# Kernel optimization log

Hardware: AMD Instinct MI355X
Metric: run time of the kernel (lower is better)

The kernel has to match this reference:

```python
import jax, jax.numpy as jnp
import numpy as np

N_BLADES = 8  # Cl(3,0): 1, e1, e2, e3 and their products (bitmask blade indexing)


def _blade_sign(a: int, b: int) -> int:
    # Sign from reordering basis vectors when multiplying blades a*b (Euclidean metric).
    a >>= 1
    s = 0
    while a:
        s += bin(a & b).count('1')
        a >>= 1
    return -1 if (s & 1) else 1


def make_cayley() -> np.ndarray:
    C = np.zeros((N_BLADES, N_BLADES, N_BLADES), dtype=np.float32)
    for a in range(N_BLADES):
        for b in range(N_BLADES):
            C[a, b, a ^ b] = float(_blade_sign(a, b))
    return C


def setup_inputs() -> dict:
    key = jax.random.key(0)
    k1, k2 = jax.random.split(key)
    B, Cin, Cout = 8192, 256, 256
    scale = 1.0 / np.sqrt(Cin * N_BLADES)
    x = jax.random.normal(k1, (B, Cin, N_BLADES), dtype=jnp.float32)
    weight = jax.random.normal(k2, (Cout, Cin, N_BLADES), dtype=jnp.float32) * scale
    bias = jnp.zeros((Cout, N_BLADES), dtype=jnp.float32)
    cayley = jnp.asarray(make_cayley())
    return {"x": x, "weight": weight, "bias": bias, "cayley": cayley}


def reference(x, weight, bias, cayley):
    # A[b,o,j,k] = sum_i W[o,i,j] * X[b,i,k]  (weight blade j times input blade k)
    A = jnp.einsum('oij,bik->bojk', weight, x)
    # Contract blade pair (j,k) into output blade l via sparse Cayley table.
    out = jnp.einsum('jkl,bojk->bol', cayley, A)
    return out + bias[None, :, :]
```

## Files before the change

### kernel.cpp

```cpp
#include <hip/hip_runtime.h>
#include <stdint.h>
#include <stddef.h>


typedef __bf16 bf16x4 __attribute__((ext_vector_type(4)));
typedef __bf16 bf16x8 __attribute__((ext_vector_type(8)));
typedef float  f32x4  __attribute__((ext_vector_type(4)));
typedef float  f32x16 __attribute__((ext_vector_type(16)));

#define BM 256
#define BN 256
#define NSLICES 64
#define SLOT 8192

__device__ __forceinline__ void async_copy16(void* lds_dst, const void* g_src) {
    __builtin_amdgcn_global_load_lds(
        (__attribute__((address_space(1))) void*)g_src,
        (__attribute__((address_space(3))) void*)lds_dst,
        16, 0, 0);
}

__global__ __launch_bounds__(256) void prep_kernel(
    const float* __restrict__ x, __bf16* __restrict__ Xb2,
    const float* __restrict__ W, const float* __restrict__ cayley,
    __bf16* __restrict__ Wt2, int M, int N, int K, int Cin, int castBlocks)
{
    if ((int)blockIdx.x < castBlocks) {
        __shared__ __bf16 T[16 * 520];
        const int tk = blockIdx.x & 15;
        const int tm = blockIdx.x >> 4;
        const int row0 = tm * 64, k0 = tk * 128;
        #pragma unroll
        for (int it = 0; it < 8; ++it) {
            int idx = threadIdx.x + it * 256;
            int r = idx >> 5, kq = idx & 31;
            f32x4 v = *(const f32x4*)(x + (size_t)(row0 + r) * K + k0 + kq * 4);
            bf16x4 b;
            b[0] = (__bf16)v[0]; b[1] = (__bf16)v[1];
            b[2] = (__bf16)v[2]; b[3] = (__bf16)v[3];
            *(bf16x4*)&T[(kq >> 1) * 520 + r * 8 + (kq & 1) * 4] = b;
        }
        __syncthreads();
        const size_t obase = (size_t)(row0 >> 8) * K * 256
                           + (size_t)(k0 >> 3) * 2048
                           + (size_t)(row0 & 255) * 8;
        #pragma unroll
        for (int it = 0; it < 4; ++it) {
            int u = threadIdx.x + it * 256;
            int koL = u >> 6, rowi = u & 63;
            bf16x8 val = *(const bf16x8*)&T[koL * 520 + rowi * 8];
            *(bf16x8*)(Xb2 + obase + (size_t)koL * 2048 + rowi * 8) = val;
        }
        return;
    }
    __shared__ float Cay[512];
    for (int t = threadIdx.x; t < 512; t += 256) Cay[t] = cayley[t];
    __syncthreads();

    int flat = ((int)blockIdx.x - castBlocks) * 256 + threadIdx.x;
    if (flat >= Cin * N) return;
    int n = flat % N;
    int i = flat / N;
    int o = n >> 3, l = n & 7;

    const float* wrow = W + ((size_t)o * Cin + i) * 8;
    float w8[8];
    #pragma unroll
    for (int j = 0; j < 8; ++j) w8[j] = wrow[j];

    bf16x8 outv;
    #pragma unroll
    for (int k = 0; k < 8; ++k) {
        float s = 0.f;
        #pragma unroll
        for (int j = 0; j < 8; ++j) s += Cay[j * 64 + k * 8 + l] * w8[j];
        outv[k] = (__bf16)s;
    }
    *(bf16x8*)(Wt2 + (size_t)(n >> 8) * K * 256 + (size_t)i * 2048
                   + (n & 255) * 8) = outv;
}

__global__ __launch_bounds__(512, 2) void gemm_bt_kernel(
    const __bf16* __restrict__ A2,
    const __bf16* __restrict__ B2,
    const float*  __restrict__ bias,
    float* __restrict__ C,
    int M, int N, int K)
{
    __shared__ __align__(16) __bf16 As[4][SLOT];
    __shared__ __align__(16) __bf16 Bs[4][SLOT];

    const int tid  = threadIdx.x;
    const int wave = tid >> 6;
    const int lane = tid & 63;
    const int l31  = lane & 31;
    const int lhi  = lane >> 5;

    const int bid = blockIdx.x;
    const int xcd = bid & 7;
    const int idx = bid >> 3;
    const int mBase = (xcd * 4 + (idx & 3)) * BM;
    const int nBase = (idx >> 2) * BN;

    const int c0 = 2 * wave, c1 = 2 * wave + 1;
    const __bf16* gA0 = A2 + (size_t)mBase * K + c0 * 512 + lane * 8;
    const __bf16* gA1 = A2 + (size_t)mBase * K + c1 * 512 + lane * 8;
    const __bf16* gB0 = B2 + (size_t)nBase * K + c0 * 512 + lane * 8;
    const __bf16* gB1 = B2 + (size_t)nBase * K + c1 * 512 + lane * 8;
    const int dstA0 = c0 * 512, dstA1 = c1 * 512;

#define STAGE_A(slot, q) do {                                              \
        async_copy16(&As[slot][dstA0], gA0 + (size_t)(q) * 8192);          \
        async_copy16(&As[slot][dstA1], gA1 + (size_t)(q) * 8192);          \
    } while (0)
#define STAGE_B(slot, q) do {                                              \
        async_copy16(&Bs[slot][dstA0], gB0 + (size_t)(q) * 8192);          \
        async_copy16(&Bs[slot][dstA1], gB1 + (size_t)(q) * 8192);          \
    } while (0)

    const int wm = wave >> 2;
    const int wn = wave & 3;
    const __bf16* paBase = &As[0][lhi * 2048 + (wm * 128 + l31) * 8];
    const __bf16* pbBase = &Bs[0][lhi * 2048 + (wn * 64  + l31) * 8];

    f32x16 acc[4][2] = {};
    bf16x8 a0A[4], b0A[2], a0B[4], b0B[2], af1[4], bf1[2];

    STAGE_A(0, 0); STAGE_B(0, 0);
    STAGE_A(1, 1); STAGE_B(1, 1);
    STAGE_A(2, 2); STAGE_B(2, 2);
    asm volatile("s_waitcnt vmcnt(8)" ::: "memory");
    __builtin_amdgcn_s_barrier();

    #pragma unroll
    for (int j = 0; j < 4; ++j)
        a0A[j] = *(const bf16x8*)(paBase + j * 256);
    #pragma unroll
    for (int q = 0; q < 2; ++q)
        b0A[q] = *(const bf16x8*)(pbBase + q * 256);

#define SLICE_BODY(s_, c_, n_, A0F, B0F, A0N, B0N, DOA, DOB, DOPF, VM0)        \
    do {                                                                       \
        _Pragma("unroll")                                                      \
        for (int j = 0; j < 4; ++j)                                            \
            af1[j] = *(const bf16x8*)(paBase + (c_) * SLOT + 4096 + j * 256);  \
        _Pragma("unroll")                                                      \
        for (int q = 0; q < 2; ++q)                                            \
            bf1[q] = *(const bf16x8*)(pbBase + (c_) * SLOT + 4096 + q * 256);  \
        if (DOA) STAGE_A(((s_) + 3) & 3, (s_) + 3);                            \
        __builtin_amdgcn_s_setprio(1);                                         \
        _Pragma("unroll")                                                      \
        for (int j = 0; j < 4; ++j)                                            \
            _Pragma("unroll")                                                  \
            for (int q = 0; q < 2; ++q)                                        \
                acc[j][q] = __builtin_amdgcn_mfma_f32_32x32x16_bf16(           \
                    A0F[j], B0F[q], acc[j][q], 0, 0, 0);                       \
        __builtin_amdgcn_s_setprio(0);                                         \
        if (VM0) asm volatile("s_waitcnt vmcnt(0)" ::: "memory");              \
        else     asm volatile("s_waitcnt vmcnt(6)" ::: "memory");              \
        __builtin_amdgcn_s_barrier();                                          \
        if (DOPF) {                                                            \
            _Pragma("unroll")                                                  \
            for (int j = 0; j < 4; ++j)                                        \
                A0N[j] = *(const bf16x8*)(paBase + (n_) * SLOT + j * 256);     \
            _Pragma("unroll")                                                  \
            for (int q = 0; q < 2; ++q)                                        \
                B0N[q] = *(const bf16x8*)(pbBase + (n_) * SLOT + q * 256);     \
        }                                                                      \
        if (DOB) STAGE_B(((s_) + 3) & 3, (s_) + 3);                            \
        __builtin_amdgcn_s_setprio(1);                                         \
        _Pragma("unroll")                                                      \
        for (int j = 0; j < 4; ++j)                                            \
            _Pragma("unroll")                                                  \
            for (int q = 0; q < 2; ++q)                                        \
                acc[j][q] = __builtin_amdgcn_mfma_f32_32x32x16_bf16(           \
                    af1[j], bf1[q], acc[j][q], 0, 0, 0);                       \
        __builtin_amdgcn_s_setprio(0);                                         \
        __builtin_amdgcn_s_barrier();                                          \
    } while (0)

    #pragma unroll 1
    for (int s4 = 0; s4 < 15; ++s4) {
        const int s = s4 * 4;
        SLICE_BODY(s + 0, 0, 1, a0A, b0A, a0B, b0B, true, true, true, false);
        SLICE_BODY(s + 1, 1, 2, a0B, b0B, a0A, b0A, true, true, true, false);
        SLICE_BODY(s + 2, 2, 3, a0A, b0A, a0B, b0B, true, true, true, false);
        SLICE_BODY(s + 3, 3, 0, a0B, b0B, a0A, b0A, true, true, true, false);
    }
    SLICE_BODY(60, 0, 1, a0A, b0A, a0B, b0B, true,  true,  true,  false);
    SLICE_BODY(61, 1, 2, a0B, b0B, a0A, b0A, false, false, true,  true);
    SLICE_BODY(62, 2, 3, a0A, b0A, a0B, b0B, false, false, true,  true);
    SLICE_BODY(63, 3, 0, a0B, b0B, a0A, b0A, false, false, false, true);
    asm volatile("s_waitcnt vmcnt(0)" ::: "memory");

#undef SLICE_BODY
#undef STAGE_A
#undef STAGE_B

    float bv[2];
    #pragma unroll
    for (int q = 0; q < 2; ++q)
        bv[q] = bias[nBase + wn * 64 + q * 32 + l31];

    #pragma unroll
    for (int mt = 0; mt < 4; ++mt) {
        #pragma unroll
        for (int q = 0; q < 2; ++q) {
            const int col = nBase + wn * 64 + q * 32 + l31;
            #pragma unroll
            for (int r = 0; r < 16; ++r) {
                const int row = mBase + wm * 128 + mt * 32
                              + (r & 3) + 8 * (r >> 2) + 4 * lhi;
                C[(size_t)row * N + col] = acc[mt][q][r] + bv[q];
            }
        }
    }
}

extern "C" void kernel_launch(void* const* d_in, const int* in_sizes, int n_in,
                              void* d_out, int out_size, void* d_ws, size_t ws_size,
                              hipStream_t stream) {
    const float* x      = (const float*)d_in[0];
    const float* weight = (const float*)d_in[1];
    const float* bias   = (const float*)d_in[2];
    const float* cayley = (const float*)d_in[3];
    float* out = (float*)d_out;

    const int Cout = in_sizes[2] / 8;
    const int Cin  = in_sizes[1] / (Cout * 8);
    const int Bm   = in_sizes[0] / (Cin * 8);
    const int M = Bm;
    const int N = Cout * 8;
    const int K = Cin * 8;

    __bf16* Xb2 = (__bf16*)d_ws;
    __bf16* Wt2 = (__bf16*)((char*)d_ws + (size_t)M * K * 2);

    int castBlocks = (M / 64) * (K / 128);
    int foldBlocks = (Cin * N + 255) / 256;
    prep_kernel<<<castBlocks + foldBlocks, 256, 0, stream>>>(
        x, Xb2, weight, cayley, Wt2, M, N, K, Cin, castBlocks);

    int grid = (M / BM) * (N / BN);
    gemm_bt_kernel<<<grid, 512, 0, stream>>>(Xb2, Wt2, bias, out, M, N, K);
}
```

Baseline: 181.7 us.

## Fuse fp32-to-bf16 activation cast into GEMM A-tile loading

Removes the separate cast/relayout pass over x and instead has the GEMM load fp32 x directly into registers, convert to bf16 and write into the LDS A tiles, with the software pipeline reworked around register-staged loads. The fold kernel is restructured to stage weights through shared memory per block. This drops a full write and re-read of the bf16 activation copy but adds conversion work, register pressure and twice the A-side global traffic per GEMM block, since fp32 is reread by each of the 8 N-tiles.

```diff
diff --git a/kernel.cpp b/kernel.cpp
--- a/kernel.cpp
+++ b/kernel.cpp
@@ -3,14 +3,12 @@
 #include <stddef.h>
 
 
-typedef __bf16 bf16x4 __attribute__((ext_vector_type(4)));
 typedef __bf16 bf16x8 __attribute__((ext_vector_type(8)));
 typedef float  f32x4  __attribute__((ext_vector_type(4)));
 typedef float  f32x16 __attribute__((ext_vector_type(16)));
 
 #define BM 256
 #define BN 256
-#define NSLICES 64
 #define SLOT 8192
 
 __device__ __forceinline__ void async_copy16(void* lds_dst, const void* g_src) {
@@ -20,53 +18,39 @@
         16, 0, 0);
 }
 
-__global__ __launch_bounds__(256) void prep_kernel(
-    const float* __restrict__ x, __bf16* __restrict__ Xb2,
+__device__ __forceinline__ bf16x8 cvt2(f32x4 a, f32x4 b) {
+    bf16x8 r;
+    r[0] = (__bf16)a[0]; r[1] = (__bf16)a[1];
+    r[2] = (__bf16)a[2]; r[3] = (__bf16)a[3];
+    r[4] = (__bf16)b[0]; r[5] = (__bf16)b[1];
+    r[6] = (__bf16)b[2]; r[7] = (__bf16)b[3];
+    return r;
+}
+
+__global__ __launch_bounds__(256) void fold_kernel(
     const float* __restrict__ W, const float* __restrict__ cayley,
-    __bf16* __restrict__ Wt2, int M, int N, int K, int Cin, int castBlocks)
+    __bf16* __restrict__ Wt2, int Cin, int N, int K)
 {
-    if ((int)blockIdx.x < castBlocks) {
-        __shared__ __bf16 T[16 * 520];
-        const int tk = blockIdx.x & 15;
-        const int tm = blockIdx.x >> 4;
-        const int row0 = tm * 64, k0 = tk * 128;
-        #pragma unroll
-        for (int it = 0; it < 8; ++it) {
-            int idx = threadIdx.x + it * 256;
-            int r = idx >> 5, kq = idx & 31;
-            f32x4 v = *(const f32x4*)(x + (size_t)(row0 + r) * K + k0 + kq * 4);
-            bf16x4 b;
-            b[0] = (__bf16)v[0]; b[1] = (__bf16)v[1];
-            b[2] = (__bf16)v[2]; b[3] = (__bf16)v[3];
-            *(bf16x4*)&T[(kq >> 1) * 520 + r * 8 + (kq & 1) * 4] = b;
-        }
-        __syncthreads();
-        const size_t obase = (size_t)(row0 >> 8) * K * 256
-                           + (size_t)(k0 >> 3) * 2048
-                           + (size_t)(row0 & 255) * 8;
-        #pragma unroll
-        for (int it = 0; it < 4; ++it) {
-            int u = threadIdx.x + it * 256;
-            int koL = u >> 6, rowi = u & 63;
-            bf16x8 val = *(const bf16x8*)&T[koL * 520 + rowi * 8];
-            *(bf16x8*)(Xb2 + obase + (size_t)koL * 2048 + rowi * 8) = val;
-        }
-        return;
-    }
     __shared__ float Cay[512];
+    __shared__ float Wl[32][8];
+    const int b  = blockIdx.x;
+    const int i  = b >> 3;
+    const int n0 = (b & 7) * 256;
+    const int o0 = n0 >> 3;
+
     for (int t = threadIdx.x; t < 512; t += 256) Cay[t] = cayley[t];
+    if (threadIdx.x < 64) {
+        int o2 = threadIdx.x >> 1, half = threadIdx.x & 1;
+        *(f32x4*)&Wl[o2][half * 4] =
+            *(const f32x4*)(W + ((size_t)(o0 + o2) * Cin + i) * 8 + half * 4);
+    }
     __syncthreads();
 
-    int flat = ((int)blockIdx.x - castBlocks) * 256 + threadIdx.x;
-    if (flat >= Cin * N) return;
-    int n = flat % N;
-    int i = flat / N;
-    int o = n >> 3, l = n & 7;
-
-    const float* wrow = W + ((size_t)o * Cin + i) * 8;
+    const int t  = threadIdx.x;
+    const int o2 = t >> 3, l = t & 7;
     float w8[8];
     #pragma unroll
-    for (int j = 0; j < 8; ++j) w8[j] = wrow[j];
+    for (int j = 0; j < 8; ++j) w8[j] = Wl[o2][j];
 
     bf16x8 outv;
     #pragma unroll
@@ -76,12 +60,13 @@
         for (int j = 0; j < 8; ++j) s += Cay[j * 64 + k * 8 + l] * w8[j];
         outv[k] = (__bf16)s;
     }
-    *(bf16x8*)(Wt2 + (size_t)(n >> 8) * K * 256 + (size_t)i * 2048
-                   + (n & 255) * 8) = outv;
+    const int n = n0 + t;
+    *(bf16x8*)(Wt2 + (size_t)(n >> 8) * (size_t)K * 256
+                   + (size_t)i * 2048 + (size_t)(n & 255) * 8) = outv;
 }
 
 __global__ __launch_bounds__(512, 2) void gemm_bt_kernel(
-    const __bf16* __restrict__ A2,
+    const float*  __restrict__ X,
     const __bf16* __restrict__ B2,
     const float*  __restrict__ bias,
     float* __restrict__ C,
@@ -102,20 +87,30 @@
     const int mBase = (xcd * 4 + (idx & 3)) * BM;
     const int nBase = (idx >> 2) * BN;
 
+    const int arow = tid >> 1;
+    const int akh  = tid & 1;
+    const float* gX = X + (size_t)(mBase + arow) * K + akh * 16;
+    const int wd0 = (2 * akh) * 2048 + arow * 8;
+    const int wd1 = wd0 + 2048;
+
     const int c0 = 2 * wave, c1 = 2 * wave + 1;
-    const __bf16* gA0 = A2 + (size_t)mBase * K + c0 * 512 + lane * 8;
-    const __bf16* gA1 = A2 + (size_t)mBase * K + c1 * 512 + lane * 8;
     const __bf16* gB0 = B2 + (size_t)nBase * K + c0 * 512 + lane * 8;
     const __bf16* gB1 = B2 + (size_t)nBase * K + c1 * 512 + lane * 8;
-    const int dstA0 = c0 * 512, dstA1 = c1 * 512;
-
-#define STAGE_A(slot, q) do {                                              \
-        async_copy16(&As[slot][dstA0], gA0 + (size_t)(q) * 8192);          \
-        async_copy16(&As[slot][dstA1], gA1 + (size_t)(q) * 8192);          \
+    const int dstB0 = c0 * 512, dstB1 = c1 * 512;
+
+#define ISSUE_A(SET, q) do {                                   \
+        SET[0] = *(const f32x4*)(gX + (size_t)(q) * 32);       \
+        SET[1] = *(const f32x4*)(gX + (size_t)(q) * 32 + 4);   \
+        SET[2] = *(const f32x4*)(gX + (size_t)(q) * 32 + 8);   \
+        SET[3] = *(const f32x4*)(gX + (size_t)(q) * 32 + 12);  \
+    } while (0)
+#define CVT_WRITE(SET, slot) do {                              \
+        *(bf16x8*)&As[slot][wd0] = cvt2(SET[0], SET[1]);       \
+        *(bf16x8*)&As[slot][wd1] = cvt2(SET[2], SET[3]);       \
     } while (0)
 #define STAGE_B(slot, q) do {                                              \
-        async_copy16(&Bs[slot][dstA0], gB0 + (size_t)(q) * 8192);          \
-        async_copy16(&Bs[slot][dstA1], gB1 + (size_t)(q) * 8192);          \
+        async_copy16(&Bs[slot][dstB0], gB0 + (size_t)(q) * 8192);          \
+        async_copy16(&Bs[slot][dstB1], gB1 + (size_t)(q) * 8192);          \
     } while (0)
 
     const int wm = wave >> 2;
@@ -125,11 +120,18 @@
 
     f32x16 acc[4][2] = {};
     bf16x8 a0A[4], b0A[2], a0B[4], b0B[2], af1[4], bf1[2];
-
-    STAGE_A(0, 0); STAGE_B(0, 0);
-    STAGE_A(1, 1); STAGE_B(1, 1);
-    STAGE_A(2, 2); STAGE_B(2, 2);
+    f32x4 aE[4], aO[4];
+
+    ISSUE_A(aE, 0); ISSUE_A(aO, 1);
+    STAGE_B(0, 0);  STAGE_B(1, 1);
     asm volatile("s_waitcnt vmcnt(8)" ::: "memory");
+    CVT_WRITE(aE, 0);
+    asm volatile("s_waitcnt vmcnt(4)" ::: "memory");
+    CVT_WRITE(aO, 1);
+    ISSUE_A(aE, 2);
+    STAGE_B(2, 2);
+    asm volatile("s_waitcnt vmcnt(6)" ::: "memory");
+    asm volatile("s_waitcnt lgkmcnt(0)" ::: "memory");
     __builtin_amdgcn_s_barrier();
 
     #pragma unroll
@@ -139,7 +141,8 @@
     for (int q = 0; q < 2; ++q)
         b0A[q] = *(const bf16x8*)(pbBase + q * 256);
 
-#define SLICE_BODY(s_, c_, n_, A0F, B0F, A0N, B0N, DOA, DOB, DOPF, VM0)        \
+#define SLICE_BODY(s_, c_, n_, A0F, B0F, A0N, B0N, AIS, ACV,                   \
+                   DOA, DOCVT, DOPF, DOB, VMODE)                               \
     do {                                                                       \
         _Pragma("unroll")                                                      \
         for (int j = 0; j < 4; ++j)                                            \
@@ -147,7 +150,7 @@
         _Pragma("unroll")                                                      \
         for (int q = 0; q < 2; ++q)                                            \
             bf1[q] = *(const bf16x8*)(pbBase + (c_) * SLOT + 4096 + q * 256);  \
-        if (DOA) STAGE_A(((s_) + 3) & 3, (s_) + 3);                            \
+        if (DOA) ISSUE_A(AIS, (s_) + 3);                                       \
         __builtin_amdgcn_s_setprio(1);                                         \
         _Pragma("unroll")                                                      \
         for (int j = 0; j < 4; ++j)                                            \
@@ -156,9 +159,12 @@
                 acc[j][q] = __builtin_amdgcn_mfma_f32_32x32x16_bf16(           \
                     A0F[j], B0F[q], acc[j][q], 0, 0, 0);                       \
         __builtin_amdgcn_s_setprio(0);                                         \
-        if (VM0) asm volatile("s_waitcnt vmcnt(0)" ::: "memory");              \
-        else     asm volatile("s_waitcnt vmcnt(6)" ::: "memory");              \
         __builtin_amdgcn_s_barrier();                                          \
+        if ((VMODE) == 0) asm volatile("s_waitcnt vmcnt(6)" ::: "memory");     \
+        else if ((VMODE) == 1) asm volatile("s_waitcnt vmcnt(2)" ::: "memory");\
+        else if ((VMODE) == 2) asm volatile("s_waitcnt vmcnt(0)" ::: "memory");\
+        if (DOB) STAGE_B(((s_) + 3) & 3, (s_) + 3);                            \
+        if (DOCVT) CVT_WRITE(ACV, ((s_) + 2) & 3);                             \
         if (DOPF) {                                                            \
             _Pragma("unroll")                                                  \
             for (int j = 0; j < 4; ++j)                                        \
@@ -167,7 +173,6 @@
             for (int q = 0; q < 2; ++q)                                        \
                 B0N[q] = *(const bf16x8*)(pbBase + (n_) * SLOT + q * 256);     \
         }                                                                      \
-        if (DOB) STAGE_B(((s_) + 3) & 3, (s_) + 3);                            \
         __builtin_amdgcn_s_setprio(1);                                         \
         _Pragma("unroll")                                                      \
         for (int j = 0; j < 4; ++j)                                            \
@@ -176,26 +181,27 @@
                 acc[j][q] = __builtin_amdgcn_mfma_f32_32x32x16_bf16(           \
                     af1[j], bf1[q], acc[j][q], 0, 0, 0);                       \
         __builtin_amdgcn_s_setprio(0);                                         \
+        asm volatile("s_waitcnt lgkmcnt(0)" ::: "memory");                     \
         __builtin_amdgcn_s_barrier();                                          \
     } while (0)
 
     #pragma unroll 1
     for (int s4 = 0; s4 < 15; ++s4) {
         const int s = s4 * 4;
-        SLICE_BODY(s + 0, 0, 1, a0A, b0A, a0B, b0B, true, true, true, false);
-        SLICE_BODY(s + 1, 1, 2, a0B, b0B, a0A, b0A, true, true, true, false);
-        SLICE_BODY(s + 2, 2, 3, a0A, b0A, a0B, b0B, true, true, true, false);
-        SLICE_BODY(s + 3, 3, 0, a0B, b0B, a0A, b0A, true, true, true, false);
-    }
-    SLICE_BODY(60, 0, 1, a0A, b0A, a0B, b0B, true,  true,  true,  false);
-    SLICE_BODY(61, 1, 2, a0B, b0B, a0A, b0A, false, false, true,  true);
-    SLICE_BODY(62, 2, 3, a0A, b0A, a0B, b0B, false, false, true,  true);
-    SLICE_BODY(63, 3, 0, a0B, b0B, a0A, b0A, false, false, false, true);
-    asm volatile("s_waitcnt vmcnt(0)" ::: "memory");
+        SLICE_BODY(s + 0, 0, 1, a0A, b0A, a0B, b0B, aO, aE, true, true, true, true, 0);
+        SLICE_BODY(s + 1, 1, 2, a0B, b0B, a0A, b0A, aE, aO, true, true, true, true, 0);
+        SLICE_BODY(s + 2, 2, 3, a0A, b0A, a0B, b0B, aO, aE, true, true, true, true, 0);
+        SLICE_BODY(s + 3, 3, 0, a0B, b0B, a0A, b0A, aE, aO, true, true, true, true, 0);
+    }
+    SLICE_BODY(60, 0, 1, a0A, b0A, a0B, b0B, aO, aE, true,  true,  true,  true,  0);
+    SLICE_BODY(61, 1, 2, a0B, b0B, a0A, b0A, aE, aO, false, true,  true,  false, 1);
+    SLICE_BODY(62, 2, 3, a0A, b0A, a0B, b0B, aO, aE, false, false, true,  false, 2);
+    SLICE_BODY(63, 3, 0, a0B, b0B, a0A, b0A, aE, aO, false, false, false, false, 3);
 
 #undef SLICE_BODY
-#undef STAGE_A
 #undef STAGE_B
+#undef CVT_WRITE
+#undef ISSUE_A
 
     float bv[2];
     #pragma unroll
@@ -233,14 +239,11 @@
     const int N = Cout * 8;
     const int K = Cin * 8;
 
-    __bf16* Xb2 = (__bf16*)d_ws;
-    __bf16* Wt2 = (__bf16*)((char*)d_ws + (size_t)M * K * 2);
-
-    int castBlocks = (M / 64) * (K / 128);
-    int foldBlocks = (Cin * N + 255) / 256;
-    prep_kernel<<<castBlocks + foldBlocks, 256, 0, stream>>>(
-        x, Xb2, weight, cayley, Wt2, M, N, K, Cin, castBlocks);
+    __bf16* Wt2 = (__bf16*)d_ws;
+
+    int foldBlocks = Cin * (N / 256);
+    fold_kernel<<<foldBlocks, 256, 0, stream>>>(weight, cayley, Wt2, Cin, N, K);
 
     int grid = (M / BM) * (N / BN);
-    gemm_bt_kernel<<<grid, 512, 0, stream>>>(Xb2, Wt2, bias, out, M, N, K);
-}
+    gemm_bt_kernel<<<grid, 512, 0, stream>>>(x, Wt2, bias, out, M, N, K);
+}
```

New measurement: 197.1 us. +8.5%, slower.
